# Optimization experiments

Hardware: AMD Instinct MI355X
Metric: run time of the kernel (lower is better)

The kernel has to match this reference:

```python
import jax, jax.numpy as jnp
import numpy as np

T, B, D = 256, 64, 512


def setup_inputs() -> dict:
    key = jax.random.key(0)
    ks = jax.random.split(key, 9)
    s = 1.0 / np.sqrt(D)  # torch Linear default init scale (uniform), use scaled normal
    return {
        "x": jax.random.normal(ks[0], (T, B, D), dtype=jnp.float32),
        "y": jax.random.normal(ks[1], (T, B, D), dtype=jnp.float32),
        "Wr": jax.random.normal(ks[2], (D, D), dtype=jnp.float32) * s,
        "Ur": jax.random.normal(ks[3], (D, D), dtype=jnp.float32) * s,
        "Wz": jax.random.normal(ks[4], (D, D), dtype=jnp.float32) * s,
        "Uz": jax.random.normal(ks[5], (D, D), dtype=jnp.float32) * s,
        "Wg": jax.random.normal(ks[6], (D, D), dtype=jnp.float32) * s,
        "Ug": jax.random.normal(ks[7], (D, D), dtype=jnp.float32) * s,
        "bg": jnp.full((D,), 2.0, dtype=jnp.float32),
    }


def reference(x, y, Wr, Ur, Wz, Uz, Wg, Ug, bg):
    # GTrXL gating unit. torch Linear(y) == y @ W.T
    r = jax.nn.sigmoid(jnp.einsum("tbd,ed->tbe", y, Wr) + jnp.einsum("tbd,ed->tbe", x, Ur))
    z = jax.nn.sigmoid(jnp.einsum("tbd,ed->tbe", y, Wz) + jnp.einsum("tbd,ed->tbe", x, Uz) - bg)
    h = jnp.tanh(jnp.einsum("tbd,ed->tbe", y, Wg) + jnp.einsum("tbd,ed->tbe", r * x, Ug))
    g = (1.0 - z) * x + z * h  # (T, B, D)
    return g
```

## Files before the change

### kernel.cpp

```cpp
#include <hip/hip_runtime.h>
#include <stdint.h>

typedef unsigned short u16;
typedef __attribute__((ext_vector_type(8))) __bf16 bf16x8;
typedef __attribute__((ext_vector_type(4))) float f32x4;

#define Dn 512
#define Mn 16384


__device__ __forceinline__ u16 f2bf(float f) {
  unsigned u = __float_as_uint(f);
  u += 0x7fffu + ((u >> 16) & 1u);
  return (u16)(u >> 16);
}

__device__ __forceinline__ float bf2f(u16 b) {
  return __uint_as_float(((unsigned)b) << 16);
}

__device__ __forceinline__ void async16(const u16* g, u16* l) {
  __builtin_amdgcn_global_load_lds(
      (const __attribute__((address_space(1))) unsigned int*)g,
      (__attribute__((address_space(3))) unsigned int*)l, 16, 0, 0);
}

__device__ __forceinline__ float sigmoidf_(float v) {
  return 1.f / (1.f + __expf(-v));
}

__global__ void cast_all2(const float* __restrict__ y, const float* __restrict__ x,
                          const float* w0, const float* w1, const float* w2,
                          const float* w3, const float* w4, const float* w5,
                          u16* __restrict__ yb, u16* __restrict__ xb,
                          u16* __restrict__ bRZ, u16* __restrict__ bG) {
  const int stride = gridDim.x * 256;
  for (int idx = blockIdx.x * 256 + (int)threadIdx.x; idx < 17920 * 256; idx += stride) {
    int b = idx >> 8;
    const int t = idx & 255;
    if (b < 16384) {
      const float* src;
      u16* dst;
      if (b < 8192) { src = y; dst = yb; }
      else          { src = x; dst = xb; b -= 8192; }
      const int i4 = b * 256 + t;
      float4 v = ((const float4*)src)[i4];
      ushort4 o;
      o.x = f2bf(v.x); o.y = f2bf(v.y); o.z = f2bf(v.z); o.w = f2bf(v.w);
      ((ushort4*)dst)[i4] = o;
      continue;
    }
    b -= 16384;
    const int wi = b >> 8;
    const int bb = b & 255;
    const float* src = wi == 0 ? w0 : wi == 1 ? w1 : wi == 2 ? w2
                     : wi == 3 ? w3 : wi == 4 ? w4 : w5;
    const int i4 = bb * 256 + t;
    const int e  = i4 >> 7;
    const int c4 = i4 & 127;
    float4 v = ((const float4*)src)[i4];
    ushort4 o;
    o.x = f2bf(v.x); o.y = f2bf(v.y); o.z = f2bf(v.z); o.w = f2bf(v.w);
    ushort4* base = (wi >= 4) ? (ushort4*)bG : (ushort4*)bRZ;
    const int row = e + ((wi == 2 || wi == 3) ? 512 : 0);
    const int off = row * 256 + c4 + ((wi & 1) ? 128 : 0);
    base[off] = o;
  }
}

__global__ __launch_bounds__(256, 4) void gemm_rz1(
    const u16* __restrict__ yb, const u16* __restrict__ xb,
    const u16* __restrict__ bRZ, const float* __restrict__ bg,
    u16* __restrict__ rxb, u16* __restrict__ zb) {
  __shared__ u16 smem[16384];
  u16* sA = smem;
  u16* sB = smem + 8192;

  const int tid = threadIdx.x;
  const int lane = tid & 63;
  const int wave = tid >> 6;
  const int waveM = wave >> 1, waveN = wave & 1;
  const int mb = blockIdx.x & 127, nb = blockIdx.x >> 7;
  const int rowStart = mb * 128, colStart = nb * 128;
  const int wbyte = (tid & 192) * 16;
  const int lm = lane & 15, quad = lane >> 4;

  const int srow = tid >> 3;
  const int scol = (((tid & 7) ^ ((tid >> 3) & 7)) * 8);
  const int lswz = lm & 7;

  f32x4 acc[4][4] = {};

  for (int kq = 0; kq < 16; ++kq) {
    const int half = kq >> 3;
    const int k0 = (kq & 7) * 64;
    const u16* abase = half ? xb : yb;
#pragma unroll
    for (int s = 0; s < 4; ++s) {
      async16(abase + (size_t)(rowStart + s * 32 + srow) * 512 + k0 + scol,
              (u16*)((char*)sA + s * 4096 + wbyte));
      async16(bRZ + (size_t)(colStart + s * 32 + srow) * 1024 + kq * 64 + scol,
              (u16*)((char*)sB + s * 4096 + wbyte));
    }
    __syncthreads();

#pragma unroll
    for (int kk = 0; kk < 2; ++kk) {
      bf16x8 aa[4], bw[4];
#pragma unroll
      for (int i = 0; i < 4; ++i)
        aa[i] = *(const bf16x8*)(sA + (waveM * 64 + i * 16 + lm) * 64 +
                                 ((kk * 4 + quad) ^ lswz) * 8);
#pragma unroll
      for (int j = 0; j < 4; ++j)
        bw[j] = *(const bf16x8*)(sB + (waveN * 64 + j * 16 + lm) * 64 +
                                 ((kk * 4 + quad) ^ lswz) * 8);
#pragma unroll
      for (int i = 0; i < 4; ++i)
#pragma unroll
        for (int j = 0; j < 4; ++j)
          acc[i][j] = __builtin_amdgcn_mfma_f32_16x16x32_bf16(aa[i], bw[j], acc[i][j], 0, 0, 0);
    }
    __syncthreads();
  }

  if (colStart < 512) {
#pragma unroll
    for (int j = 0; j < 4; ++j) {
      const int e = colStart + waveN * 64 + j * 16 + lm;
#pragma unroll
      for (int i = 0; i < 4; ++i) {
        const int m0 = rowStart + waveM * 64 + i * 16 + quad * 4;
#pragma unroll
        for (int rg = 0; rg < 4; ++rg) {
          const size_t idx = (size_t)(m0 + rg) * 512 + e;
          const float r = sigmoidf_(acc[i][j][rg]);
          rxb[idx] = f2bf(r * bf2f(xb[idx]));
        }
      }
    }
  } else {
#pragma unroll
    for (int j = 0; j < 4; ++j) {
      const int e = colStart - 512 + waveN * 64 + j * 16 + lm;
      const float bgv = bg[e];
#pragma unroll
      for (int i = 0; i < 4; ++i) {
        const int m0 = rowStart + waveM * 64 + i * 16 + quad * 4;
#pragma unroll
        for (int rg = 0; rg < 4; ++rg) {
          const size_t idx = (size_t)(m0 + rg) * 512 + e;
          zb[idx] = f2bf(sigmoidf_(acc[i][j][rg] - bgv));
        }
      }
    }
  }
}

__global__ __launch_bounds__(256, 4) void gemm_gu2(
    const u16* __restrict__ yb, const u16* __restrict__ rxb,
    const u16* __restrict__ bG,
    const u16* __restrict__ zb, const u16* __restrict__ xb,
    float* __restrict__ out) {
  __shared__ u16 smem[12288];
  u16* sA = smem;
  u16* sB = smem + 4096;

  const int tid = threadIdx.x;
  const int lane = tid & 63;
  const int wave = tid >> 6;
  const int waveM = wave >> 1, waveN = wave & 1;
  const int mb = blockIdx.x & 255, nb = blockIdx.x >> 8;
  const int rowStart = mb * 64, colStart = nb * 128;
  const int wbyte = (tid & 192) * 16;
  const int lm = lane & 15, quad = lane >> 4;

  const int srow = tid >> 3;
  const int scol = (((tid & 7) ^ ((tid >> 3) & 7)) * 8);
  const int lswz = lm & 7;

  f32x4 acc[2][4] = {};

  for (int kq = 0; kq < 16; ++kq) {
    const int half = kq >> 3;
    const int k0 = (kq & 7) * 64;
    const u16* abase = half ? rxb : yb;
#pragma unroll
    for (int s = 0; s < 2; ++s)
      async16(abase + (size_t)(rowStart + s * 32 + srow) * 512 + k0 + scol,
              (u16*)((char*)sA + s * 4096 + wbyte));
#pragma unroll
    for (int s = 0; s < 4; ++s)
      async16(bG + (size_t)(colStart + s * 32 + srow) * 1024 + kq * 64 + scol,
              (u16*)((char*)sB + s * 4096 + wbyte));
    __syncthreads();

#pragma unroll
    for (int kk = 0; kk < 2; ++kk) {
      bf16x8 aa[2], bw[4];
#pragma unroll
      for (int i = 0; i < 2; ++i)
        aa[i] = *(const bf16x8*)(sA + (waveM * 32 + i * 16 + lm) * 64 +
                                 ((kk * 4 + quad) ^ lswz) * 8);
#pragma unroll
      for (int j = 0; j < 4; ++j)
        bw[j] = *(const bf16x8*)(sB + (waveN * 64 + j * 16 + lm) * 64 +
                                 ((kk * 4 + quad) ^ lswz) * 8);
#pragma unroll
      for (int i = 0; i < 2; ++i)
#pragma unroll
        for (int j = 0; j < 4; ++j)
          acc[i][j] = __builtin_amdgcn_mfma_f32_16x16x32_bf16(aa[i], bw[j], acc[i][j], 0, 0, 0);
    }
    __syncthreads();
  }

#pragma unroll
  for (int j = 0; j < 4; ++j) {
    const int e = colStart + waveN * 64 + j * 16 + lm;
#pragma unroll
    for (int i = 0; i < 2; ++i) {
      const int m0 = rowStart + waveM * 32 + i * 16 + quad * 4;
#pragma unroll
      for (int rg = 0; rg < 4; ++rg) {
        const size_t idx = (size_t)(m0 + rg) * 512 + e;
        const float pre = acc[i][j][rg];
        const float ex = __expf(-2.f * pre);
        const float h = (1.f - ex) / (1.f + ex);
        const float z = bf2f(zb[idx]);
        const float xv = bf2f(xb[idx]);
        out[idx] = (1.f - z) * xv + z * h;
      }
    }
  }
}

extern "C" void kernel_launch(void* const* d_in, const int* in_sizes, int n_in,
                              void* d_out, int out_size, void* d_ws, size_t ws_size,
                              hipStream_t stream) {
  const float* x  = (const float*)d_in[0];
  const float* y  = (const float*)d_in[1];
  const float* Wr = (const float*)d_in[2];
  const float* Ur = (const float*)d_in[3];
  const float* Wz = (const float*)d_in[4];
  const float* Uz = (const float*)d_in[5];
  const float* Wg = (const float*)d_in[6];
  const float* Ug = (const float*)d_in[7];
  const float* bg = (const float*)d_in[8];
  float* out = (float*)d_out;

  char* ws = (char*)d_ws;
  u16* yb  = (u16*)(ws);
  u16* xb  = (u16*)(ws + 16777216);
  u16* rxb = (u16*)(ws + 2 * 16777216);
  u16* zb  = (u16*)(ws + 3 * 16777216);
  u16* bRZ = (u16*)(ws + 4 * 16777216);
  u16* bG  = (u16*)(ws + 4 * 16777216 + 2097152);

  cast_all2<<<2048, 256, 0, stream>>>(y, x, Wr, Ur, Wz, Uz, Wg, Ug, yb, xb, bRZ, bG);
  gemm_rz1<<<1024, 256, 0, stream>>>(yb, xb, bRZ, bg, rxb, zb);
  gemm_gu2<<<1024, 256, 0, stream>>>(yb, rxb, bG, zb, xb, out);
}
```

Before: 203.4 us.

## Fuse cast and both GEMM stages into one persistent kernel with grid barriers

Merges the three launches (bf16 cast, r/z GEMM, g GEMM with output blend) into a single kernel of 1024 blocks that separates the phases with a software grid-wide barrier built on agent-scope atomics. The aim is to remove launch gaps and per-kernel tail effects. It relies on all 1024 blocks being co-resident (4 per CU under the launch bounds, which needs enough CUs). It also adds a memset before each launch and a spin-wait with a timeout that could silently break the barrier.

```diff
diff --git a/kernel.cpp b/kernel.cpp
--- a/kernel.cpp
+++ b/kernel.cpp
@@ -7,6 +7,7 @@
 
 #define Dn 512
 #define Mn 16384
+#define GRID_BLOCKS 1024u
 
 
 __device__ __forceinline__ u16 f2bf(float f) {
@@ -29,207 +30,227 @@
   return 1.f / (1.f + __expf(-v));
 }
 
-__global__ void cast_all2(const float* __restrict__ y, const float* __restrict__ x,
-                          const float* w0, const float* w1, const float* w2,
-                          const float* w3, const float* w4, const float* w5,
-                          u16* __restrict__ yb, u16* __restrict__ xb,
-                          u16* __restrict__ bRZ, u16* __restrict__ bG) {
-  const int stride = gridDim.x * 256;
-  for (int idx = blockIdx.x * 256 + (int)threadIdx.x; idx < 17920 * 256; idx += stride) {
-    int b = idx >> 8;
-    const int t = idx & 255;
-    if (b < 16384) {
-      const float* src;
-      u16* dst;
-      if (b < 8192) { src = y; dst = yb; }
-      else          { src = x; dst = xb; b -= 8192; }
-      const int i4 = b * 256 + t;
+__device__ __forceinline__ void grid_barrier(unsigned* cnt, unsigned* gen) {
+  __syncthreads();
+  if (threadIdx.x == 0) {
+    __threadfence();
+    unsigned g = __hip_atomic_load(gen, __ATOMIC_RELAXED, __HIP_MEMORY_SCOPE_AGENT);
+    unsigned arrived = __hip_atomic_fetch_add(cnt, 1u, __ATOMIC_ACQ_REL, __HIP_MEMORY_SCOPE_AGENT);
+    if (arrived == GRID_BLOCKS - 1u) {
+      __hip_atomic_store(cnt, 0u, __ATOMIC_RELAXED, __HIP_MEMORY_SCOPE_AGENT);
+      __hip_atomic_store(gen, g + 1u, __ATOMIC_RELEASE, __HIP_MEMORY_SCOPE_AGENT);
+    } else {
+      unsigned spins = 0;
+      while (__hip_atomic_load(gen, __ATOMIC_ACQUIRE, __HIP_MEMORY_SCOPE_AGENT) == g) {
+        __builtin_amdgcn_s_sleep(2);
+        if (++spins > (1u << 23)) break;
+      }
+    }
+    __threadfence();
+  }
+  __syncthreads();
+}
+
+struct FArgs {
+  const float *y, *x, *w0, *w1, *w2, *w3, *w4, *w5, *bg;
+  u16 *yb, *xb, *rxb, *zb, *bRZ, *bG;
+  float* out;
+  unsigned *bar_cnt, *bar_gen;
+};
+
+__global__ __launch_bounds__(256, 4) void fused_gru(FArgs a) {
+  __shared__ u16 smem[16384];
+  const int tid = (int)threadIdx.x;
+
+  {
+    const int stride = (int)gridDim.x * 256;
+    for (int idx = (int)blockIdx.x * 256 + tid; idx < 17920 * 256; idx += stride) {
+      int b = idx >> 8;
+      const int t = idx & 255;
+      if (b < 16384) {
+        const float* src;
+        u16* dst;
+        if (b < 8192) { src = a.y; dst = a.yb; }
+        else          { src = a.x; dst = a.xb; b -= 8192; }
+        const int i4 = b * 256 + t;
+        float4 v = ((const float4*)src)[i4];
+        ushort4 o;
+        o.x = f2bf(v.x); o.y = f2bf(v.y); o.z = f2bf(v.z); o.w = f2bf(v.w);
+        ((ushort4*)dst)[i4] = o;
+        continue;
+      }
+      b -= 16384;
+      const int wi = b >> 8;
+      const int bb = b & 255;
+      const float* src = wi == 0 ? a.w0 : wi == 1 ? a.w1 : wi == 2 ? a.w2
+                       : wi == 3 ? a.w3 : wi == 4 ? a.w4 : a.w5;
+      const int i4 = bb * 256 + t;
+      const int e  = i4 >> 7;
+      const int c4 = i4 & 127;
       float4 v = ((const float4*)src)[i4];
       ushort4 o;
       o.x = f2bf(v.x); o.y = f2bf(v.y); o.z = f2bf(v.z); o.w = f2bf(v.w);
-      ((ushort4*)dst)[i4] = o;
-      continue;
-    }
-    b -= 16384;
-    const int wi = b >> 8;
-    const int bb = b & 255;
-    const float* src = wi == 0 ? w0 : wi == 1 ? w1 : wi == 2 ? w2
-                     : wi == 3 ? w3 : wi == 4 ? w4 : w5;
-    const int i4 = bb * 256 + t;
-    const int e  = i4 >> 7;
-    const int c4 = i4 & 127;
-    float4 v = ((const float4*)src)[i4];
-    ushort4 o;
-    o.x = f2bf(v.x); o.y = f2bf(v.y); o.z = f2bf(v.z); o.w = f2bf(v.w);
-    ushort4* base = (wi >= 4) ? (ushort4*)bG : (ushort4*)bRZ;
-    const int row = e + ((wi == 2 || wi == 3) ? 512 : 0);
-    const int off = row * 256 + c4 + ((wi & 1) ? 128 : 0);
-    base[off] = o;
-  }
-}
-
-__global__ __launch_bounds__(256, 4) void gemm_rz1(
-    const u16* __restrict__ yb, const u16* __restrict__ xb,
-    const u16* __restrict__ bRZ, const float* __restrict__ bg,
-    u16* __restrict__ rxb, u16* __restrict__ zb) {
-  __shared__ u16 smem[16384];
-  u16* sA = smem;
-  u16* sB = smem + 8192;
-
-  const int tid = threadIdx.x;
-  const int lane = tid & 63;
-  const int wave = tid >> 6;
-  const int waveM = wave >> 1, waveN = wave & 1;
-  const int mb = blockIdx.x & 127, nb = blockIdx.x >> 7;
-  const int rowStart = mb * 128, colStart = nb * 128;
-  const int wbyte = (tid & 192) * 16;
-  const int lm = lane & 15, quad = lane >> 4;
-
-  const int srow = tid >> 3;
-  const int scol = (((tid & 7) ^ ((tid >> 3) & 7)) * 8);
-  const int lswz = lm & 7;
-
-  f32x4 acc[4][4] = {};
-
-  for (int kq = 0; kq < 16; ++kq) {
-    const int half = kq >> 3;
-    const int k0 = (kq & 7) * 64;
-    const u16* abase = half ? xb : yb;
-#pragma unroll
-    for (int s = 0; s < 4; ++s) {
-      async16(abase + (size_t)(rowStart + s * 32 + srow) * 512 + k0 + scol,
-              (u16*)((char*)sA + s * 4096 + wbyte));
-      async16(bRZ + (size_t)(colStart + s * 32 + srow) * 1024 + kq * 64 + scol,
-              (u16*)((char*)sB + s * 4096 + wbyte));
-    }
-    __syncthreads();
-
-#pragma unroll
-    for (int kk = 0; kk < 2; ++kk) {
-      bf16x8 aa[4], bw[4];
-#pragma unroll
-      for (int i = 0; i < 4; ++i)
-        aa[i] = *(const bf16x8*)(sA + (waveM * 64 + i * 16 + lm) * 64 +
-                                 ((kk * 4 + quad) ^ lswz) * 8);
-#pragma unroll
-      for (int j = 0; j < 4; ++j)
-        bw[j] = *(const bf16x8*)(sB + (waveN * 64 + j * 16 + lm) * 64 +
-                                 ((kk * 4 + quad) ^ lswz) * 8);
-#pragma unroll
-      for (int i = 0; i < 4; ++i)
+      ushort4* base = (wi >= 4) ? (ushort4*)a.bG : (ushort4*)a.bRZ;
+      const int row = e + ((wi == 2 || wi == 3) ? 512 : 0);
+      const int off = row * 256 + c4 + ((wi & 1) ? 128 : 0);
+      base[off] = o;
+    }
+  }
+  grid_barrier(a.bar_cnt, a.bar_gen);
+
+  {
+    u16* sA = smem;
+    u16* sB = smem + 8192;
+
+    const int lane = tid & 63;
+    const int wave = tid >> 6;
+    const int waveM = wave >> 1, waveN = wave & 1;
+    const int mb = (int)blockIdx.x & 127, nb = (int)blockIdx.x >> 7;
+    const int rowStart = mb * 128, colStart = nb * 128;
+    const int wbyte = (tid & 192) * 16;
+    const int lm = lane & 15, quad = lane >> 4;
+
+    const int srow = tid >> 3;
+    const int scol = (((tid & 7) ^ ((tid >> 3) & 7)) * 8);
+    const int lswz = lm & 7;
+
+    f32x4 acc[4][4] = {};
+
+    for (int kq = 0; kq < 16; ++kq) {
+      const int half = kq >> 3;
+      const int k0 = (kq & 7) * 64;
+      const u16* abase = half ? a.xb : a.yb;
+#pragma unroll
+      for (int s = 0; s < 4; ++s) {
+        async16(abase + (size_t)(rowStart + s * 32 + srow) * 512 + k0 + scol,
+                (u16*)((char*)sA + s * 4096 + wbyte));
+        async16(a.bRZ + (size_t)(colStart + s * 32 + srow) * 1024 + kq * 64 + scol,
+                (u16*)((char*)sB + s * 4096 + wbyte));
+      }
+      __syncthreads();
+
+#pragma unroll
+      for (int kk = 0; kk < 2; ++kk) {
+        bf16x8 aa[4], bw[4];
+#pragma unroll
+        for (int i = 0; i < 4; ++i)
+          aa[i] = *(const bf16x8*)(sA + (waveM * 64 + i * 16 + lm) * 64 +
+                                   ((kk * 4 + quad) ^ lswz) * 8);
 #pragma unroll
         for (int j = 0; j < 4; ++j)
-          acc[i][j] = __builtin_amdgcn_mfma_f32_16x16x32_bf16(aa[i], bw[j], acc[i][j], 0, 0, 0);
-    }
-    __syncthreads();
-  }
-
-  if (colStart < 512) {
+          bw[j] = *(const bf16x8*)(sB + (waveN * 64 + j * 16 + lm) * 64 +
+                                   ((kk * 4 + quad) ^ lswz) * 8);
+#pragma unroll
+        for (int i = 0; i < 4; ++i)
+#pragma unroll
+          for (int j = 0; j < 4; ++j)
+            acc[i][j] = __builtin_amdgcn_mfma_f32_16x16x32_bf16(aa[i], bw[j], acc[i][j], 0, 0, 0);
+      }
+      __syncthreads();
+    }
+
+    if (colStart < 512) {
+#pragma unroll
+      for (int j = 0; j < 4; ++j) {
+        const int e = colStart + waveN * 64 + j * 16 + lm;
+#pragma unroll
+        for (int i = 0; i < 4; ++i) {
+          const int m0 = rowStart + waveM * 64 + i * 16 + quad * 4;
+#pragma unroll
+          for (int rg = 0; rg < 4; ++rg) {
+            const size_t idx = (size_t)(m0 + rg) * 512 + e;
+            const float r = sigmoidf_(acc[i][j][rg]);
+            a.rxb[idx] = f2bf(r * bf2f(a.xb[idx]));
+          }
+        }
+      }
+    } else {
+#pragma unroll
+      for (int j = 0; j < 4; ++j) {
+        const int e = colStart - 512 + waveN * 64 + j * 16 + lm;
+        const float bgv = a.bg[e];
+#pragma unroll
+        for (int i = 0; i < 4; ++i) {
+          const int m0 = rowStart + waveM * 64 + i * 16 + quad * 4;
+#pragma unroll
+          for (int rg = 0; rg < 4; ++rg) {
+            const size_t idx = (size_t)(m0 + rg) * 512 + e;
+            a.zb[idx] = f2bf(sigmoidf_(acc[i][j][rg] - bgv));
+          }
+        }
+      }
+    }
+  }
+  grid_barrier(a.bar_cnt, a.bar_gen);
+
+  {
+    u16* sA = smem;
+    u16* sB = smem + 4096;
+
+    const int lane = tid & 63;
+    const int wave = tid >> 6;
+    const int waveM = wave >> 1, waveN = wave & 1;
+    const int mb = (int)blockIdx.x & 255, nb = (int)blockIdx.x >> 8;
+    const int rowStart = mb * 64, colStart = nb * 128;
+    const int wbyte = (tid & 192) * 16;
+    const int lm = lane & 15, quad = lane >> 4;
+
+    const int srow = tid >> 3;
+    const int scol = (((tid & 7) ^ ((tid >> 3) & 7)) * 8);
+    const int lswz = lm & 7;
+
+    f32x4 acc[2][4] = {};
+
+    for (int kq = 0; kq < 16; ++kq) {
+      const int half = kq >> 3;
+      const int k0 = (kq & 7) * 64;
+      const u16* abase = half ? a.rxb : a.yb;
+#pragma unroll
+      for (int s = 0; s < 2; ++s)
+        async16(abase + (size_t)(rowStart + s * 32 + srow) * 512 + k0 + scol,
+                (u16*)((char*)sA + s * 4096 + wbyte));
+#pragma unroll
+      for (int s = 0; s < 4; ++s)
+        async16(a.bG + (size_t)(colStart + s * 32 + srow) * 1024 + kq * 64 + scol,
+                (u16*)((char*)sB + s * 4096 + wbyte));
+      __syncthreads();
+
+#pragma unroll
+      for (int kk = 0; kk < 2; ++kk) {
+        bf16x8 aa[2], bw[4];
+#pragma unroll
+        for (int i = 0; i < 2; ++i)
+          aa[i] = *(const bf16x8*)(sA + (waveM * 32 + i * 16 + lm) * 64 +
+                                   ((kk * 4 + quad) ^ lswz) * 8);
+#pragma unroll
+        for (int j = 0; j < 4; ++j)
+          bw[j] = *(const bf16x8*)(sB + (waveN * 64 + j * 16 + lm) * 64 +
+                                   ((kk * 4 + quad) ^ lswz) * 8);
+#pragma unroll
+        for (int i = 0; i < 2; ++i)
+#pragma unroll
+          for (int j = 0; j < 4; ++j)
+            acc[i][j] = __builtin_amdgcn_mfma_f32_16x16x32_bf16(aa[i], bw[j], acc[i][j], 0, 0, 0);
+      }
+      __syncthreads();
+    }
+
 #pragma unroll
     for (int j = 0; j < 4; ++j) {
       const int e = colStart + waveN * 64 + j * 16 + lm;
 #pragma unroll
-      for (int i = 0; i < 4; ++i) {
-        const int m0 = rowStart + waveM * 64 + i * 16 + quad * 4;
+      for (int i = 0; i < 2; ++i) {
+        const int m0 = rowStart + waveM * 32 + i * 16 + quad * 4;
 #pragma unroll
         for (int rg = 0; rg < 4; ++rg) {
           const size_t idx = (size_t)(m0 + rg) * 512 + e;
-          const float r = sigmoidf_(acc[i][j][rg]);
-          rxb[idx] = f2bf(r * bf2f(xb[idx]));
+          const float pre = acc[i][j][rg];
+          const float ex = __expf(-2.f * pre);
+          const float h = (1.f - ex) / (1.f + ex);
+          const float z = bf2f(a.zb[idx]);
+          const float xv = bf2f(a.xb[idx]);
+          a.out[idx] = (1.f - z) * xv + z * h;
         }
-      }
-    }
-  } else {
-#pragma unroll
-    for (int j = 0; j < 4; ++j) {
-      const int e = colStart - 512 + waveN * 64 + j * 16 + lm;
-      const float bgv = bg[e];
-#pragma unroll
-      for (int i = 0; i < 4; ++i) {
-        const int m0 = rowStart + waveM * 64 + i * 16 + quad * 4;
-#pragma unroll
-        for (int rg = 0; rg < 4; ++rg) {
-          const size_t idx = (size_t)(m0 + rg) * 512 + e;
-          zb[idx] = f2bf(sigmoidf_(acc[i][j][rg] - bgv));
-        }
-      }
-    }
-  }
-}
-
-__global__ __launch_bounds__(256, 4) void gemm_gu2(
-    const u16* __restrict__ yb, const u16* __restrict__ rxb,
-    const u16* __restrict__ bG,
-    const u16* __restrict__ zb, const u16* __restrict__ xb,
-    float* __restrict__ out) {
-  __shared__ u16 smem[12288];
-  u16* sA = smem;
-  u16* sB = smem + 4096;
-
-  const int tid = threadIdx.x;
-  const int lane = tid & 63;
-  const int wave = tid >> 6;
-  const int waveM = wave >> 1, waveN = wave & 1;
-  const int mb = blockIdx.x & 255, nb = blockIdx.x >> 8;
-  const int rowStart = mb * 64, colStart = nb * 128;
-  const int wbyte = (tid & 192) * 16;
-  const int lm = lane & 15, quad = lane >> 4;
-
-  const int srow = tid >> 3;
-  const int scol = (((tid & 7) ^ ((tid >> 3) & 7)) * 8);
-  const int lswz = lm & 7;
-
-  f32x4 acc[2][4] = {};
-
-  for (int kq = 0; kq < 16; ++kq) {
-    const int half = kq >> 3;
-    const int k0 = (kq & 7) * 64;
-    const u16* abase = half ? rxb : yb;
-#pragma unroll
-    for (int s = 0; s < 2; ++s)
-      async16(abase + (size_t)(rowStart + s * 32 + srow) * 512 + k0 + scol,
-              (u16*)((char*)sA + s * 4096 + wbyte));
-#pragma unroll
-    for (int s = 0; s < 4; ++s)
-      async16(bG + (size_t)(colStart + s * 32 + srow) * 1024 + kq * 64 + scol,
-              (u16*)((char*)sB + s * 4096 + wbyte));
-    __syncthreads();
-
-#pragma unroll
-    for (int kk = 0; kk < 2; ++kk) {
-      bf16x8 aa[2], bw[4];
-#pragma unroll
-      for (int i = 0; i < 2; ++i)
-        aa[i] = *(const bf16x8*)(sA + (waveM * 32 + i * 16 + lm) * 64 +
-                                 ((kk * 4 + quad) ^ lswz) * 8);
-#pragma unroll
-      for (int j = 0; j < 4; ++j)
-        bw[j] = *(const bf16x8*)(sB + (waveN * 64 + j * 16 + lm) * 64 +
-                                 ((kk * 4 + quad) ^ lswz) * 8);
-#pragma unroll
-      for (int i = 0; i < 2; ++i)
-#pragma unroll
-        for (int j = 0; j < 4; ++j)
-          acc[i][j] = __builtin_amdgcn_mfma_f32_16x16x32_bf16(aa[i], bw[j], acc[i][j], 0, 0, 0);
-    }
-    __syncthreads();
-  }
-
-#pragma unroll
-  for (int j = 0; j < 4; ++j) {
-    const int e = colStart + waveN * 64 + j * 16 + lm;
-#pragma unroll
-    for (int i = 0; i < 2; ++i) {
-      const int m0 = rowStart + waveM * 32 + i * 16 + quad * 4;
-#pragma unroll
-      for (int rg = 0; rg < 4; ++rg) {
-        const size_t idx = (size_t)(m0 + rg) * 512 + e;
-        const float pre = acc[i][j][rg];
-        const float ex = __expf(-2.f * pre);
-        const float h = (1.f - ex) / (1.f + ex);
-        const float z = bf2f(zb[idx]);
-        const float xv = bf2f(xb[idx]);
-        out[idx] = (1.f - z) * xv + z * h;
       }
     }
   }
@@ -238,26 +259,28 @@
 extern "C" void kernel_launch(void* const* d_in, const int* in_sizes, int n_in,
                               void* d_out, int out_size, void* d_ws, size_t ws_size,
                               hipStream_t stream) {
-  const float* x  = (const float*)d_in[0];
-  const float* y  = (const float*)d_in[1];
-  const float* Wr = (const float*)d_in[2];
-  const float* Ur = (const float*)d_in[3];
-  const float* Wz = (const float*)d_in[4];
-  const float* Uz = (const float*)d_in[5];
-  const float* Wg = (const float*)d_in[6];
-  const float* Ug = (const float*)d_in[7];
-  const float* bg = (const float*)d_in[8];
-  float* out = (float*)d_out;
-
   char* ws = (char*)d_ws;
-  u16* yb  = (u16*)(ws);
-  u16* xb  = (u16*)(ws + 16777216);
-  u16* rxb = (u16*)(ws + 2 * 16777216);
-  u16* zb  = (u16*)(ws + 3 * 16777216);
-  u16* bRZ = (u16*)(ws + 4 * 16777216);
-  u16* bG  = (u16*)(ws + 4 * 16777216 + 2097152);
-
-  cast_all2<<<2048, 256, 0, stream>>>(y, x, Wr, Ur, Wz, Uz, Wg, Ug, yb, xb, bRZ, bG);
-  gemm_rz1<<<1024, 256, 0, stream>>>(yb, xb, bRZ, bg, rxb, zb);
-  gemm_gu2<<<1024, 256, 0, stream>>>(yb, rxb, bG, zb, xb, out);
-}
+  FArgs fa;
+  fa.x  = (const float*)d_in[0];
+  fa.y  = (const float*)d_in[1];
+  fa.w0 = (const float*)d_in[2];
+  fa.w1 = (const float*)d_in[3];
+  fa.w2 = (const float*)d_in[4];
+  fa.w3 = (const float*)d_in[5];
+  fa.w4 = (const float*)d_in[6];
+  fa.w5 = (const float*)d_in[7];
+  fa.bg = (const float*)d_in[8];
+  fa.yb  = (u16*)(ws);
+  fa.xb  = (u16*)(ws + 16777216);
+  fa.rxb = (u16*)(ws + 2 * 16777216);
+  fa.zb  = (u16*)(ws + 3 * 16777216);
+  fa.bRZ = (u16*)(ws + 4 * 16777216);
+  fa.bG  = (u16*)(ws + 4 * 16777216 + 2097152);
+  char* bar = ws + 4 * 16777216 + 2097152 + 1048576;
+  fa.bar_cnt = (unsigned*)(bar);
+  fa.bar_gen = (unsigned*)(bar + 128);
+  fa.out = (float*)d_out;
+
+  hipMemsetAsync(bar, 0, 256, stream);
+  fused_gru<<<dim3(GRID_BLOCKS), dim3(256), 0, stream>>>(fa);
+}
```

After: 611.8 us. 3.01x slower.

## Fuse RZ and G GEMMs into one kernel with per-row-block flag sync

Applied to the files above, without the earlier changes.

Merges the two GEMM launches into a single 2048-block kernel. The G-stage blocks compute the y·Wg half first, then spin on per-row-block counters set by the RZ blocks before loading r*x and z through coherent atomic loads. The aim is to overlap the second GEMM's independent half with the first GEMM and drop the kernel boundary. The cost is relaxed-atomic 16-bit stores, spin-waiting that relies on block scheduling order (with a bailout that could read stale data), and a synchronous-style LDS copy path for rxb instead of async loads.

```diff
diff --git a/kernel.cpp b/kernel.cpp
--- a/kernel.cpp
+++ b/kernel.cpp
@@ -2,6 +2,7 @@
 #include <stdint.h>
 
 typedef unsigned short u16;
+typedef unsigned long long u64;
 typedef __attribute__((ext_vector_type(8))) __bf16 bf16x8;
 typedef __attribute__((ext_vector_type(4))) float f32x4;
 
@@ -27,6 +28,16 @@
 
 __device__ __forceinline__ float sigmoidf_(float v) {
   return 1.f / (1.f + __expf(-v));
+}
+
+__device__ __forceinline__ void st_u16_coh(u16* p, u16 v) {
+  __hip_atomic_store(p, v, __ATOMIC_RELAXED, __HIP_MEMORY_SCOPE_AGENT);
+}
+__device__ __forceinline__ u16 ld_u16_coh(const u16* p) {
+  return __hip_atomic_load(p, __ATOMIC_RELAXED, __HIP_MEMORY_SCOPE_AGENT);
+}
+__device__ __forceinline__ u64 ld_u64_coh(const u64* p) {
+  return __hip_atomic_load(p, __ATOMIC_RELAXED, __HIP_MEMORY_SCOPE_AGENT);
 }
 
 __global__ void cast_all2(const float* __restrict__ y, const float* __restrict__ x,
@@ -68,168 +79,212 @@
   }
 }
 
-__global__ __launch_bounds__(256, 4) void gemm_rz1(
-    const u16* __restrict__ yb, const u16* __restrict__ xb,
-    const u16* __restrict__ bRZ, const float* __restrict__ bg,
-    u16* __restrict__ rxb, u16* __restrict__ zb) {
+struct GArgs {
+  const u16 *yb, *xb, *bRZ, *bG;
+  const float* bg;
+  u16 *rxb, *zb;
+  const u16 *rxb_c, *zb_c;
+  float* out;
+  unsigned* flags;
+};
+
+__global__ __launch_bounds__(256, 4) void gemm_rzgu(GArgs a) {
   __shared__ u16 smem[16384];
-  u16* sA = smem;
-  u16* sB = smem + 8192;
-
-  const int tid = threadIdx.x;
+  const int tid = (int)threadIdx.x;
   const int lane = tid & 63;
   const int wave = tid >> 6;
   const int waveM = wave >> 1, waveN = wave & 1;
-  const int mb = blockIdx.x & 127, nb = blockIdx.x >> 7;
-  const int rowStart = mb * 128, colStart = nb * 128;
   const int wbyte = (tid & 192) * 16;
   const int lm = lane & 15, quad = lane >> 4;
-
   const int srow = tid >> 3;
   const int scol = (((tid & 7) ^ ((tid >> 3) & 7)) * 8);
   const int lswz = lm & 7;
 
-  f32x4 acc[4][4] = {};
-
-  for (int kq = 0; kq < 16; ++kq) {
-    const int half = kq >> 3;
-    const int k0 = (kq & 7) * 64;
-    const u16* abase = half ? xb : yb;
-#pragma unroll
-    for (int s = 0; s < 4; ++s) {
-      async16(abase + (size_t)(rowStart + s * 32 + srow) * 512 + k0 + scol,
-              (u16*)((char*)sA + s * 4096 + wbyte));
-      async16(bRZ + (size_t)(colStart + s * 32 + srow) * 1024 + kq * 64 + scol,
-              (u16*)((char*)sB + s * 4096 + wbyte));
-    }
+  if (blockIdx.x < 1024) {
+    u16* sA = smem;
+    u16* sB = smem + 8192;
+    const int mb = (int)blockIdx.x & 127, nb = (int)blockIdx.x >> 7;
+    const int rowStart = mb * 128, colStart = nb * 128;
+
+    f32x4 acc[4][4] = {};
+
+    for (int kq = 0; kq < 16; ++kq) {
+      const int half = kq >> 3;
+      const int k0 = (kq & 7) * 64;
+      const u16* abase = half ? a.xb : a.yb;
+#pragma unroll
+      for (int s = 0; s < 4; ++s) {
+        async16(abase + (size_t)(rowStart + s * 32 + srow) * 512 + k0 + scol,
+                (u16*)((char*)sA + s * 4096 + wbyte));
+        async16(a.bRZ + (size_t)(colStart + s * 32 + srow) * 1024 + kq * 64 + scol,
+                (u16*)((char*)sB + s * 4096 + wbyte));
+      }
+      __syncthreads();
+
+#pragma unroll
+      for (int kk = 0; kk < 2; ++kk) {
+        bf16x8 aa[4], bw[4];
+#pragma unroll
+        for (int i = 0; i < 4; ++i)
+          aa[i] = *(const bf16x8*)(sA + (waveM * 64 + i * 16 + lm) * 64 +
+                                   ((kk * 4 + quad) ^ lswz) * 8);
+#pragma unroll
+        for (int j = 0; j < 4; ++j)
+          bw[j] = *(const bf16x8*)(sB + (waveN * 64 + j * 16 + lm) * 64 +
+                                   ((kk * 4 + quad) ^ lswz) * 8);
+#pragma unroll
+        for (int i = 0; i < 4; ++i)
+#pragma unroll
+          for (int j = 0; j < 4; ++j)
+            acc[i][j] = __builtin_amdgcn_mfma_f32_16x16x32_bf16(aa[i], bw[j], acc[i][j], 0, 0, 0);
+      }
+      __syncthreads();
+    }
+
+    if (colStart < 512) {
+#pragma unroll
+      for (int j = 0; j < 4; ++j) {
+        const int e = colStart + waveN * 64 + j * 16 + lm;
+#pragma unroll
+        for (int i = 0; i < 4; ++i) {
+          const int m0 = rowStart + waveM * 64 + i * 16 + quad * 4;
+#pragma unroll
+          for (int rg = 0; rg < 4; ++rg) {
+            const size_t idx = (size_t)(m0 + rg) * 512 + e;
+            const float r = sigmoidf_(acc[i][j][rg]);
+            st_u16_coh(&a.rxb[idx], f2bf(r * bf2f(a.xb[idx])));
+          }
+        }
+      }
+    } else {
+#pragma unroll
+      for (int j = 0; j < 4; ++j) {
+        const int e = colStart - 512 + waveN * 64 + j * 16 + lm;
+        const float bgv = a.bg[e];
+#pragma unroll
+        for (int i = 0; i < 4; ++i) {
+          const int m0 = rowStart + waveM * 64 + i * 16 + quad * 4;
+#pragma unroll
+          for (int rg = 0; rg < 4; ++rg) {
+            const size_t idx = (size_t)(m0 + rg) * 512 + e;
+            st_u16_coh(&a.zb[idx], f2bf(sigmoidf_(acc[i][j][rg] - bgv)));
+          }
+        }
+      }
+    }
+    asm volatile("s_waitcnt vmcnt(0)" ::: "memory");
     __syncthreads();
-
-#pragma unroll
-    for (int kk = 0; kk < 2; ++kk) {
-      bf16x8 aa[4], bw[4];
-#pragma unroll
-      for (int i = 0; i < 4; ++i)
-        aa[i] = *(const bf16x8*)(sA + (waveM * 64 + i * 16 + lm) * 64 +
-                                 ((kk * 4 + quad) ^ lswz) * 8);
-#pragma unroll
-      for (int j = 0; j < 4; ++j)
-        bw[j] = *(const bf16x8*)(sB + (waveN * 64 + j * 16 + lm) * 64 +
-                                 ((kk * 4 + quad) ^ lswz) * 8);
-#pragma unroll
-      for (int i = 0; i < 4; ++i)
+    if (tid == 0)
+      __hip_atomic_fetch_add(&a.flags[mb], 1u, __ATOMIC_RELAXED, __HIP_MEMORY_SCOPE_AGENT);
+    return;
+  }
+
+  {
+    u16* sA = smem;
+    u16* sB = smem + 4096;
+    const int bid2 = (int)blockIdx.x - 1024;
+    const int mb = bid2 & 255, nb = bid2 >> 8;
+    const int rowStart = mb * 64, colStart = nb * 128;
+
+    f32x4 acc[2][4] = {};
+
+    for (int kq = 0; kq < 8; ++kq) {
+      const int k0 = kq * 64;
+#pragma unroll
+      for (int s = 0; s < 2; ++s)
+        async16(a.yb + (size_t)(rowStart + s * 32 + srow) * 512 + k0 + scol,
+                (u16*)((char*)sA + s * 4096 + wbyte));
+#pragma unroll
+      for (int s = 0; s < 4; ++s)
+        async16(a.bG + (size_t)(colStart + s * 32 + srow) * 1024 + kq * 64 + scol,
+                (u16*)((char*)sB + s * 4096 + wbyte));
+      __syncthreads();
+
+#pragma unroll
+      for (int kk = 0; kk < 2; ++kk) {
+        bf16x8 aa[2], bw[4];
+#pragma unroll
+        for (int i = 0; i < 2; ++i)
+          aa[i] = *(const bf16x8*)(sA + (waveM * 32 + i * 16 + lm) * 64 +
+                                   ((kk * 4 + quad) ^ lswz) * 8);
 #pragma unroll
         for (int j = 0; j < 4; ++j)
-          acc[i][j] = __builtin_amdgcn_mfma_f32_16x16x32_bf16(aa[i], bw[j], acc[i][j], 0, 0, 0);
+          bw[j] = *(const bf16x8*)(sB + (waveN * 64 + j * 16 + lm) * 64 +
+                                   ((kk * 4 + quad) ^ lswz) * 8);
+#pragma unroll
+        for (int i = 0; i < 2; ++i)
+#pragma unroll
+          for (int j = 0; j < 4; ++j)
+            acc[i][j] = __builtin_amdgcn_mfma_f32_16x16x32_bf16(aa[i], bw[j], acc[i][j], 0, 0, 0);
+      }
+      __syncthreads();
+    }
+
+    if (tid == 0) {
+      unsigned spins = 0;
+      const int mf = mb >> 1;
+      while (__hip_atomic_load(&a.flags[mf], __ATOMIC_RELAXED, __HIP_MEMORY_SCOPE_AGENT) < 8u) {
+        __builtin_amdgcn_s_sleep(8);
+        if (++spins > (1u << 18)) break;
+      }
     }
     __syncthreads();
-  }
-
-  if (colStart < 512) {
+    asm volatile("" ::: "memory");
+    __builtin_amdgcn_sched_barrier(0);
+
+    for (int kq = 8; kq < 16; ++kq) {
+      const int k0 = (kq & 7) * 64;
+#pragma unroll
+      for (int s = 0; s < 2; ++s) {
+        const u64* src = (const u64*)(a.rxb_c + (size_t)(rowStart + s * 32 + srow) * 512 + k0 + scol);
+        u64 lo = ld_u64_coh(src);
+        u64 hi = ld_u64_coh(src + 1);
+        u64* dst = (u64*)((char*)sA + s * 4096 + wbyte + (lane << 4));
+        dst[0] = lo;
+        dst[1] = hi;
+      }
+#pragma unroll
+      for (int s = 0; s < 4; ++s)
+        async16(a.bG + (size_t)(colStart + s * 32 + srow) * 1024 + kq * 64 + scol,
+                (u16*)((char*)sB + s * 4096 + wbyte));
+      __syncthreads();
+
+#pragma unroll
+      for (int kk = 0; kk < 2; ++kk) {
+        bf16x8 aa[2], bw[4];
+#pragma unroll
+        for (int i = 0; i < 2; ++i)
+          aa[i] = *(const bf16x8*)(sA + (waveM * 32 + i * 16 + lm) * 64 +
+                                   ((kk * 4 + quad) ^ lswz) * 8);
+#pragma unroll
+        for (int j = 0; j < 4; ++j)
+          bw[j] = *(const bf16x8*)(sB + (waveN * 64 + j * 16 + lm) * 64 +
+                                   ((kk * 4 + quad) ^ lswz) * 8);
+#pragma unroll
+        for (int i = 0; i < 2; ++i)
+#pragma unroll
+          for (int j = 0; j < 4; ++j)
+            acc[i][j] = __builtin_amdgcn_mfma_f32_16x16x32_bf16(aa[i], bw[j], acc[i][j], 0, 0, 0);
+      }
+      __syncthreads();
+    }
+
 #pragma unroll
     for (int j = 0; j < 4; ++j) {
       const int e = colStart + waveN * 64 + j * 16 + lm;
 #pragma unroll
-      for (int i = 0; i < 4; ++i) {
-        const int m0 = rowStart + waveM * 64 + i * 16 + quad * 4;
+      for (int i = 0; i < 2; ++i) {
+        const int m0 = rowStart + waveM * 32 + i * 16 + quad * 4;
 #pragma unroll
         for (int rg = 0; rg < 4; ++rg) {
           const size_t idx = (size_t)(m0 + rg) * 512 + e;
-          const float r = sigmoidf_(acc[i][j][rg]);
-          rxb[idx] = f2bf(r * bf2f(xb[idx]));
+          const float pre = acc[i][j][rg];
+          const float ex = __expf(-2.f * pre);
+          const float h = (1.f - ex) / (1.f + ex);
+          const float z = bf2f(ld_u16_coh(&a.zb_c[idx]));
+          const float xv = bf2f(a.xb[idx]);
+          a.out[idx] = (1.f - z) * xv + z * h;
         }
-      }
-    }
-  } else {
-#pragma unroll
-    for (int j = 0; j < 4; ++j) {
-      const int e = colStart - 512 + waveN * 64 + j * 16 + lm;
-      const float bgv = bg[e];
-#pragma unroll
-      for (int i = 0; i < 4; ++i) {
-        const int m0 = rowStart + waveM * 64 + i * 16 + quad * 4;
-#pragma unroll
-        for (int rg = 0; rg < 4; ++rg) {
-          const size_t idx = (size_t)(m0 + rg) * 512 + e;
-          zb[idx] = f2bf(sigmoidf_(acc[i][j][rg] - bgv));
-        }
-      }
-    }
-  }
-}
-
-__global__ __launch_bounds__(256, 4) void gemm_gu2(
-    const u16* __restrict__ yb, const u16* __restrict__ rxb,
-    const u16* __restrict__ bG,
-    const u16* __restrict__ zb, const u16* __restrict__ xb,
-    float* __restrict__ out) {
-  __shared__ u16 smem[12288];
-  u16* sA = smem;
-  u16* sB = smem + 4096;
-
-  const int tid = threadIdx.x;
-  const int lane = tid & 63;
-  const int wave = tid >> 6;
-  const int waveM = wave >> 1, waveN = wave & 1;
-  const int mb = blockIdx.x & 255, nb = blockIdx.x >> 8;
-  const int rowStart = mb * 64, colStart = nb * 128;
-  const int wbyte = (tid & 192) * 16;
-  const int lm = lane & 15, quad = lane >> 4;
-
-  const int srow = tid >> 3;
-  const int scol = (((tid & 7) ^ ((tid >> 3) & 7)) * 8);
-  const int lswz = lm & 7;
-
-  f32x4 acc[2][4] = {};
-
-  for (int kq = 0; kq < 16; ++kq) {
-    const int half = kq >> 3;
-    const int k0 = (kq & 7) * 64;
-    const u16* abase = half ? rxb : yb;
-#pragma unroll
-    for (int s = 0; s < 2; ++s)
-      async16(abase + (size_t)(rowStart + s * 32 + srow) * 512 + k0 + scol,
-              (u16*)((char*)sA + s * 4096 + wbyte));
-#pragma unroll
-    for (int s = 0; s < 4; ++s)
-      async16(bG + (size_t)(colStart + s * 32 + srow) * 1024 + kq * 64 + scol,
-              (u16*)((char*)sB + s * 4096 + wbyte));
-    __syncthreads();
-
-#pragma unroll
-    for (int kk = 0; kk < 2; ++kk) {
-      bf16x8 aa[2], bw[4];
-#pragma unroll
-      for (int i = 0; i < 2; ++i)
-        aa[i] = *(const bf16x8*)(sA + (waveM * 32 + i * 16 + lm) * 64 +
-                                 ((kk * 4 + quad) ^ lswz) * 8);
-#pragma unroll
-      for (int j = 0; j < 4; ++j)
-        bw[j] = *(const bf16x8*)(sB + (waveN * 64 + j * 16 + lm) * 64 +
-                                 ((kk * 4 + quad) ^ lswz) * 8);
-#pragma unroll
-      for (int i = 0; i < 2; ++i)
-#pragma unroll
-        for (int j = 0; j < 4; ++j)
-          acc[i][j] = __builtin_amdgcn_mfma_f32_16x16x32_bf16(aa[i], bw[j], acc[i][j], 0, 0, 0);
-    }
-    __syncthreads();
-  }
-
-#pragma unroll
-  for (int j = 0; j < 4; ++j) {
-    const int e = colStart + waveN * 64 + j * 16 + lm;
-#pragma unroll
-    for (int i = 0; i < 2; ++i) {
-      const int m0 = rowStart + waveM * 32 + i * 16 + quad * 4;
-#pragma unroll
-      for (int rg = 0; rg < 4; ++rg) {
-        const size_t idx = (size_t)(m0 + rg) * 512 + e;
-        const float pre = acc[i][j][rg];
-        const float ex = __expf(-2.f * pre);
-        const float h = (1.f - ex) / (1.f + ex);
-        const float z = bf2f(zb[idx]);
-        const float xv = bf2f(xb[idx]);
-        out[idx] = (1.f - z) * xv + z * h;
       }
     }
   }
@@ -247,7 +302,6 @@
   const float* Wg = (const float*)d_in[6];
   const float* Ug = (const float*)d_in[7];
   const float* bg = (const float*)d_in[8];
-  float* out = (float*)d_out;
 
   char* ws = (char*)d_ws;
   u16* yb  = (u16*)(ws);
@@ -256,8 +310,15 @@
   u16* zb  = (u16*)(ws + 3 * 16777216);
   u16* bRZ = (u16*)(ws + 4 * 16777216);
   u16* bG  = (u16*)(ws + 4 * 16777216 + 2097152);
-
+  unsigned* flags = (unsigned*)(ws + 4 * 16777216 + 2097152 + 1048576);
+
+  GArgs ga;
+  ga.yb = yb; ga.xb = xb; ga.bRZ = bRZ; ga.bG = bG; ga.bg = bg;
+  ga.rxb = rxb; ga.zb = zb; ga.rxb_c = rxb; ga.zb_c = zb;
+  ga.out = (float*)d_out;
+  ga.flags = flags;
+
+  hipMemsetAsync(flags, 0, 512, stream);
   cast_all2<<<2048, 256, 0, stream>>>(y, x, Wr, Ur, Wz, Uz, Wg, Ug, yb, xb, bRZ, bG);
-  gemm_rz1<<<1024, 256, 0, stream>>>(yb, xb, bRZ, bg, rxb, zb);
-  gemm_gu2<<<1024, 256, 0, stream>>>(yb, rxb, bG, zb, xb, out);
-}
+  gemm_rzgu<<<2048, 256, 0, stream>>>(ga);
+}
```

Result: slower. 233.9 us (+15.0%).
